# Performance work log

Measured on AMD Instinct MI355X. Metric: run time of the kernel, lower is better.

Reference implementation:

```python
import jax, jax.numpy as jnp
import numpy as np

N = 100000   # nodes
E = 1600000  # directed edges
NF = 128     # n_feat
NH = 128     # n_hid
NC = 64      # n_class


def _glorot(key, fan_in, fan_out):
    lim = (6.0 / (fan_in + fan_out)) ** 0.5
    return jax.random.uniform(key, (fan_in, fan_out), dtype=jnp.float32, minval=-lim, maxval=lim)


def setup_inputs() -> dict:
    key = jax.random.key(0)
    ks = jax.random.split(key, 10)
    x = jax.random.normal(ks[0], (N, NF), dtype=jnp.float32)
    edge_index = jax.random.randint(ks[1], (2, E), 0, N, dtype=jnp.int32)
    return {
        "x": x,
        "edge_index": edge_index,
        "W_in": _glorot(ks[2], NF, NH),
        "b_in": jnp.zeros((NH,), jnp.float32),
        "W_mid0": _glorot(ks[3], NH, NH),
        "b_mid0": jnp.zeros((NH,), jnp.float32),
        "W_mid1": _glorot(ks[4], NH, NH),
        "b_mid1": jnp.zeros((NH,), jnp.float32),
        "W_out": _glorot(ks[5], NH, NC),
        "b_out": jnp.zeros((NC,), jnp.float32),
        "W_skip_out": _glorot(ks[6], NH, NC),
    }


def _gcn_conv(x, W, b, src, dst, coef, n):
    # x' = D^-1/2 (A + I) D^-1/2 (x W) + b   (symmetric-normalized GCN conv)
    h = x @ W                               # [N, out]
    msg = h[src] * coef[:, None]            # [E+N, out] gather + scale
    return jax.ops.segment_sum(msg, dst, num_segments=n) + b


def reference(x, edge_index, W_in, b_in, W_mid0, b_mid0, W_mid1, b_mid1, W_out, b_out, W_skip_out):
    loops = jnp.arange(N, dtype=edge_index.dtype)
    src = jnp.concatenate([edge_index[0], loops])  # add self-loops
    dst = jnp.concatenate([edge_index[1], loops])
    deg = jax.ops.segment_sum(jnp.ones_like(dst, dtype=jnp.float32), dst, num_segments=N)
    dinv = jax.lax.rsqrt(deg)                      # deg >= 1 due to self-loops
    coef = dinv[src] * dinv[dst]                   # [E+N]

    # in layer: conv + res skip (NF == NH so plain add) + relu; dropout is no-op in eval
    h = _gcn_conv(x, W_in, b_in, src, dst, coef, N)
    x = jax.nn.relu(h + x)
    # mid layers
    for W, b in ((W_mid0, b_mid0), (W_mid1, b_mid1)):
        h = _gcn_conv(x, W, b, src, dst, coef, N)
        x = jax.nn.relu(h + x)
    # out layer: conv + res skip with channel projection NH -> NC
    h = _gcn_conv(x, W_out, b_out, src, dst, coef, N)
    return h + x @ W_skip_out
```

## Files before the change

### kernel.cpp

```cpp
#include <hip/hip_runtime.h>
#include <hip/hip_bf16.h>

constexpr int NN = 100000;
constexpr int NE = 1600000;
constexpr int BKN  = 256;
constexpr int NB2  = (NN + BKN - 1) / BKN;
constexpr int TILE = 4096;
constexpr int NT   = (NE + TILE - 1) / TILE;

__device__ __forceinline__ unsigned short f2bf(float f) {
    unsigned int u = __float_as_uint(f);
    unsigned int r = (u + 0x7fffu + ((u >> 16) & 1u)) >> 16;
    return (unsigned short)r;
}
__device__ __forceinline__ float bflo(unsigned int u) { return __uint_as_float(u << 16); }
__device__ __forceinline__ float bfhi(unsigned int u) { return __uint_as_float(u & 0xffff0000u); }
__device__ __forceinline__ float bf2f(unsigned short h) { return __uint_as_float(((unsigned int)h) << 16); }
__device__ __forceinline__ unsigned int pack2bf(float lo, float hi) {
    return (unsigned int)f2bf(lo) | ((unsigned int)f2bf(hi) << 16);
}

typedef __bf16 v8bf __attribute__((ext_vector_type(8)));
typedef float  v4f  __attribute__((ext_vector_type(4)));
typedef float  v2f  __attribute__((ext_vector_type(2)));

__device__ __forceinline__ v2f fp8x2_to_f32(unsigned int u) {
    return __builtin_amdgcn_cvt_pk_f32_fp8(u, false);
}

constexpr size_t OFF_BCNT  = 0;
constexpr size_t OFF_BBASE = OFF_BCNT  + 2048;
constexpr size_t OFF_BCUR  = OFF_BBASE + 2048;
constexpr size_t OFF_RP    = OFF_BCUR  + 2048;
constexpr size_t OFF_DINV  = OFF_RP    + 400384;
constexpr size_t OFF_COL   = OFF_DINV  + 400384;
constexpr size_t OFF_WT    = OFF_COL   + 6400000;
constexpr size_t OFF_H8    = OFF_WT    + 32768;
constexpr size_t OFF_H     = OFF_H8    + 12800000;
constexpr size_t OFF_X     = OFF_H     + 25600000;


__global__ __launch_bounds__(256) void bhist_kernel(const int* __restrict__ edst,
                                                    int* __restrict__ bcnt) {
    __shared__ int h[NB2];
    for (int i = threadIdx.x; i < NB2; i += 256) h[i] = 0;
    __syncthreads();
    const int base = blockIdx.x * TILE;
    #pragma unroll
    for (int j = 0; j < 16; ++j) {
        int e = base + j * 256 + threadIdx.x;
        if (e < NE) atomicAdd(&h[edst[e] >> 8], 1);
    }
    __syncthreads();
    for (int i = threadIdx.x; i < NB2; i += 256)
        if (h[i]) atomicAdd(&bcnt[i], h[i]);
}

__global__ __launch_bounds__(512) void bscan_kernel(const int* __restrict__ bcnt,
                                                    int* __restrict__ bbase,
                                                    int* __restrict__ bcur) {
    __shared__ int s[512];
    const int t = threadIdx.x;
    int v = (t < NB2) ? bcnt[t] : 0;
    s[t] = v;
    __syncthreads();
    for (int off = 1; off < 512; off <<= 1) {
        int a = (t >= off) ? s[t - off] : 0;
        __syncthreads();
        s[t] += a;
        __syncthreads();
    }
    int excl = s[t] - v;
    if (t < NB2) { bbase[t] = excl; bcur[t] = excl; }
    if (t == NB2 - 1) bbase[NB2] = excl + v;
}

__global__ __launch_bounds__(256) void scatter2_kernel(const int* __restrict__ esrc,
                                                       const int* __restrict__ edst,
                                                       int* __restrict__ bcur,
                                                       unsigned int* __restrict__ ebuf) {
    __shared__ int h[NB2];
    __shared__ int cur[NB2];
    for (int i = threadIdx.x; i < NB2; i += 256) h[i] = 0;
    __syncthreads();
    const int base = blockIdx.x * TILE;
    #pragma unroll
    for (int j = 0; j < 16; ++j) {
        int e = base + j * 256 + threadIdx.x;
        if (e < NE) atomicAdd(&h[edst[e] >> 8], 1);
    }
    __syncthreads();
    for (int i = threadIdx.x; i < NB2; i += 256) {
        int c = h[i];
        cur[i] = c ? atomicAdd(&bcur[i], c) : 0;
    }
    __syncthreads();
    #pragma unroll
    for (int j = 0; j < 16; ++j) {
        int e = base + j * 256 + threadIdx.x;
        if (e < NE) {
            int s = esrc[e], d = edst[e];
            int pos = atomicAdd(&cur[d >> 8], 1);
            ebuf[pos] = (unsigned int)s | ((unsigned int)(d & 255) << 24);
        }
    }
}

__global__ __launch_bounds__(256) void csrfill2_kernel(const unsigned int* __restrict__ ebuf,
                                                       const int* __restrict__ bbase,
                                                       int* __restrict__ rp,
                                                       float* __restrict__ dinv,
                                                       int* __restrict__ col) {
    __shared__ int cnt[256];
    __shared__ int cursor[256];
    __shared__ int s[256];
    __shared__ int sbeg, send;
    const int b = blockIdx.x;
    const int t = threadIdx.x;
    if (t == 0) { sbeg = bbase[b]; send = bbase[b + 1]; }
    cnt[t] = 0;
    __syncthreads();
    const int beg = sbeg, end = send;
    const int node0 = b * BKN;

    for (int e = beg + t; e < end; e += 256)
        atomicAdd(&cnt[ebuf[e] >> 24], 1);
    __syncthreads();

    int v = cnt[t];
    s[t] = v;
    __syncthreads();
    for (int off = 1; off < 256; off <<= 1) {
        int a = (t >= off) ? s[t - off] : 0;
        __syncthreads();
        s[t] += a;
        __syncthreads();
    }
    int excl = s[t] - v;
    int gnode = node0 + t;
    if (gnode < NN) {
        rp[gnode]   = beg + excl;
        dinv[gnode] = rsqrtf((float)(v + 1));
    }
    cursor[t] = beg + excl;
    if (b == NB2 - 1 && t == 0) rp[NN] = NE;
    __syncthreads();

    for (int e = beg + t; e < end; e += 256) {
        unsigned int sd = ebuf[e];
        int pos = atomicAdd(&cursor[sd >> 24], 1);
        col[pos] = (int)(sd & 0xFFFFFFu);
    }
}

__global__ __launch_bounds__(256) void wpre_kernel(const float* __restrict__ W0,
                                                   const float* __restrict__ W1,
                                                   int wstride,
                                                   unsigned short* __restrict__ Wt) {
    int e = blockIdx.x * 256 + threadIdx.x;
    int k = e >> 7, c = e & 127;
    float v = (c < 64) ? W0[(size_t)k * wstride + c] : W1[(size_t)k * wstride + (c - 64)];
    Wt[c * 128 + k] = f2bf(v);
}

constexpr int XROW = 136;

template<bool XF32, bool OUT8>
__global__ __launch_bounds__(256) void gemm_mfma_kernel(const void* __restrict__ Xv,
                                                        const unsigned short* __restrict__ Wt,
                                                        const float* __restrict__ dinv,
                                                        int scaleMask,
                                                        void* __restrict__ Ho) {
    __shared__ unsigned short Wl[128 * XROW];
    __shared__ unsigned short Xl[64 * XROW];

    const int t = threadIdx.x;
    const int rowBase = blockIdx.x * 64;

    #pragma unroll
    for (int i = 0; i < 8; ++i) {
        int f = i * 256 + t;
        int r = f >> 4, c8 = f & 15;
        uint4 w = *(const uint4*)&Wt[r * 128 + c8 * 8];
        *(uint4*)&Wl[r * XROW + c8 * 8] = w;
    }
    if (XF32) {
        const float* X = (const float*)Xv;
        #pragma unroll
        for (int i = 0; i < 8; ++i) {
            int f = i * 256 + t;
            int r = f >> 5, c4 = f & 31;
            int gn = rowBase + r;
            float4 v = make_float4(0.f, 0.f, 0.f, 0.f);
            if (gn < NN) v = *(const float4*)&X[(size_t)gn * 128 + c4 * 4];
            ushort4 o;
            o.x = f2bf(v.x); o.y = f2bf(v.y); o.z = f2bf(v.z); o.w = f2bf(v.w);
            *(ushort4*)&Xl[r * XROW + c4 * 4] = o;
        }
    } else {
        const unsigned short* X = (const unsigned short*)Xv;
        #pragma unroll
        for (int i = 0; i < 4; ++i) {
            int f = i * 256 + t;
            int r = f >> 4, c8 = f & 15;
            int gn = rowBase + r;
            uint4 v = make_uint4(0u, 0u, 0u, 0u);
            if (gn < NN) v = *(const uint4*)&X[(size_t)gn * 128 + c8 * 8];
            *(uint4*)&Xl[r * XROW + c8 * 8] = v;
        }
    }
    __syncthreads();

    const int w  = t >> 6;
    const int l  = t & 63;
    const int lr = l & 15;
    const int lk = (l >> 4) * 8;

    v4f acc[8];
    #pragma unroll
    for (int n = 0; n < 8; ++n) acc[n] = (v4f){0.f, 0.f, 0.f, 0.f};

    const unsigned short* ax = &Xl[(w * 16 + lr) * XROW + lk];
    const unsigned short* bx = &Wl[lr * XROW + lk];

    #pragma unroll
    for (int kk = 0; kk < 4; ++kk) {
        v8bf a = *(const v8bf*)&ax[kk * 32];
        #pragma unroll
        for (int n = 0; n < 8; ++n) {
            v8bf b = *(const v8bf*)&bx[(n * 16) * XROW + kk * 32];
            acc[n] = __builtin_amdgcn_mfma_f32_16x16x32_bf16(a, b, acc[n], 0, 0, 0);
        }
    }

    #pragma unroll
    for (int r_ = 0; r_ < 4; ++r_) {
        int row  = w * 16 + (l >> 4) * 4 + r_;
        int grow = rowBase + row;
        float dsc = dinv[grow < NN ? grow : NN - 1];
        #pragma unroll
        for (int n = 0; n < 8; ++n) {
            float sc = ((scaleMask >> (n >> 2)) & 1) ? dsc : 1.f;
            Xl[row * XROW + n * 16 + lr] = f2bf(acc[n][r_] * sc);
        }
    }
    __syncthreads();

    if (OUT8) {
        unsigned char* H8 = (unsigned char*)Ho;
        #pragma unroll
        for (int i = 0; i < 4; ++i) {
            int f = i * 256 + t;
            int r = f >> 4, c8 = f & 15;
            int gn = rowBase + r;
            if (gn < NN) {
                uint4 v = *(const uint4*)&Xl[r * XROW + c8 * 8];
                unsigned int lo = __builtin_amdgcn_cvt_pk_fp8_f32(bflo(v.x), bfhi(v.x), 0u, false);
                lo = __builtin_amdgcn_cvt_pk_fp8_f32(bflo(v.y), bfhi(v.y), lo, true);
                unsigned int hi = __builtin_amdgcn_cvt_pk_fp8_f32(bflo(v.z), bfhi(v.z), 0u, false);
                hi = __builtin_amdgcn_cvt_pk_fp8_f32(bflo(v.w), bfhi(v.w), hi, true);
                *(uint2*)&H8[(size_t)gn * 128 + c8 * 8] = make_uint2(lo, hi);
            }
        }
    } else {
        unsigned short* Hb = (unsigned short*)Ho;
        #pragma unroll
        for (int i = 0; i < 4; ++i) {
            int f = i * 256 + t;
            int r = f >> 4, c8 = f & 15;
            int gn = rowBase + r;
            if (gn < NN) {
                uint4 v = *(const uint4*)&Xl[r * XROW + c8 * 8];
                *(uint4*)&Hb[(size_t)gn * 128 + c8 * 8] = v;
            }
        }
    }
}

template<bool XF32>
__global__ __launch_bounds__(256) void agg128_kernel(const unsigned char* __restrict__ H8,
                                                     const void* __restrict__ Xoldv,
                                                     const int* __restrict__ rp,
                                                     const int* __restrict__ col,
                                                     const float* __restrict__ dinv,
                                                     const float* __restrict__ bias,
                                                     unsigned int* __restrict__ Xnew) {
    const int wid  = threadIdx.x >> 6;
    const int lane = threadIdx.x & 63;
    const int i = blockIdx.x * 4 + wid;
    if (i >= NN) return;

    const unsigned short* __restrict__ Hs = (const unsigned short*)H8;

    const float di = dinv[i];
    const float2 b2 = ((const float2*)bias)[lane];
    float xox, xoy;
    if (XF32) {
        float2 xo = ((const float2*)Xoldv)[(size_t)i * 64 + lane];
        xox = xo.x; xoy = xo.y;
    } else {
        unsigned int xo = ((const unsigned int*)Xoldv)[(size_t)i * 64 + lane];
        xox = bflo(xo); xoy = bfhi(xo);
    }

    v2f sf = fp8x2_to_f32(Hs[(size_t)i * 64 + lane]);
    float ax = sf.x, ay = sf.y;

    const int beg = rp[i], end = rp[i + 1];
    int e = beg;
    for (; e + 8 <= end; e += 8) {
        int s0 = col[e],     s1 = col[e + 1], s2 = col[e + 2], s3 = col[e + 3];
        int s4 = col[e + 4], s5 = col[e + 5], s6 = col[e + 6], s7 = col[e + 7];
        unsigned int u0 = Hs[(size_t)s0 * 64 + lane];
        unsigned int u1 = Hs[(size_t)s1 * 64 + lane];
        unsigned int u2 = Hs[(size_t)s2 * 64 + lane];
        unsigned int u3 = Hs[(size_t)s3 * 64 + lane];
        unsigned int u4 = Hs[(size_t)s4 * 64 + lane];
        unsigned int u5 = Hs[(size_t)s5 * 64 + lane];
        unsigned int u6 = Hs[(size_t)s6 * 64 + lane];
        unsigned int u7 = Hs[(size_t)s7 * 64 + lane];
        v2f m0 = fp8x2_to_f32(u0), m1 = fp8x2_to_f32(u1);
        v2f m2 = fp8x2_to_f32(u2), m3 = fp8x2_to_f32(u3);
        v2f m4 = fp8x2_to_f32(u4), m5 = fp8x2_to_f32(u5);
        v2f m6 = fp8x2_to_f32(u6), m7 = fp8x2_to_f32(u7);
        ax += ((m0.x + m1.x) + (m2.x + m3.x)) + ((m4.x + m5.x) + (m6.x + m7.x));
        ay += ((m0.y + m1.y) + (m2.y + m3.y)) + ((m4.y + m5.y) + (m6.y + m7.y));
    }
    for (; e + 4 <= end; e += 4) {
        int s0 = col[e], s1 = col[e + 1], s2 = col[e + 2], s3 = col[e + 3];
        unsigned int u0 = Hs[(size_t)s0 * 64 + lane];
        unsigned int u1 = Hs[(size_t)s1 * 64 + lane];
        unsigned int u2 = Hs[(size_t)s2 * 64 + lane];
        unsigned int u3 = Hs[(size_t)s3 * 64 + lane];
        v2f m0 = fp8x2_to_f32(u0), m1 = fp8x2_to_f32(u1);
        v2f m2 = fp8x2_to_f32(u2), m3 = fp8x2_to_f32(u3);
        ax += (m0.x + m1.x) + (m2.x + m3.x);
        ay += (m0.y + m1.y) + (m2.y + m3.y);
    }
    for (; e < end; ++e) {
        v2f m = fp8x2_to_f32(Hs[(size_t)col[e] * 64 + lane]);
        ax += m.x;
        ay += m.y;
    }

    float ox = fmaxf(di * ax + b2.x + xox, 0.f);
    float oy = fmaxf(di * ay + b2.y + xoy, 0.f);
    Xnew[(size_t)i * 64 + lane] = pack2bf(ox, oy);
}

__global__ __launch_bounds__(256) void aggout_kernel(const unsigned short* __restrict__ Hb,
                                                     const int* __restrict__ rp,
                                                     const int* __restrict__ col,
                                                     const float* __restrict__ dinv,
                                                     const float* __restrict__ bias,
                                                     float* __restrict__ out) {
    const int wid  = threadIdx.x >> 6;
    const int lane = threadIdx.x & 63;
    const int i = blockIdx.x * 4 + wid;
    if (i >= NN) return;

    const float di = dinv[i];
    const float b  = bias[lane];
    const float sk = bf2f(Hb[(size_t)i * 128 + 64 + lane]);

    float a = bf2f(Hb[(size_t)i * 128 + lane]);
    const int beg = rp[i], end = rp[i + 1];
    int e = beg;
    for (; e + 8 <= end; e += 8) {
        int s0 = col[e],     s1 = col[e + 1], s2 = col[e + 2], s3 = col[e + 3];
        int s4 = col[e + 4], s5 = col[e + 5], s6 = col[e + 6], s7 = col[e + 7];
        float m0 = bf2f(Hb[(size_t)s0 * 128 + lane]);
        float m1 = bf2f(Hb[(size_t)s1 * 128 + lane]);
        float m2 = bf2f(Hb[(size_t)s2 * 128 + lane]);
        float m3 = bf2f(Hb[(size_t)s3 * 128 + lane]);
        float m4 = bf2f(Hb[(size_t)s4 * 128 + lane]);
        float m5 = bf2f(Hb[(size_t)s5 * 128 + lane]);
        float m6 = bf2f(Hb[(size_t)s6 * 128 + lane]);
        float m7 = bf2f(Hb[(size_t)s7 * 128 + lane]);
        a += ((m0 + m1) + (m2 + m3)) + ((m4 + m5) + (m6 + m7));
    }
    for (; e + 4 <= end; e += 4) {
        int s0 = col[e], s1 = col[e + 1], s2 = col[e + 2], s3 = col[e + 3];
        float m0 = bf2f(Hb[(size_t)s0 * 128 + lane]);
        float m1 = bf2f(Hb[(size_t)s1 * 128 + lane]);
        float m2 = bf2f(Hb[(size_t)s2 * 128 + lane]);
        float m3 = bf2f(Hb[(size_t)s3 * 128 + lane]);
        a += (m0 + m1) + (m2 + m3);
    }
    for (; e < end; ++e) a += bf2f(Hb[(size_t)col[e] * 128 + lane]);

    out[(size_t)i * 64 + lane] = di * a + b + sk;
}

extern "C" void kernel_launch(void* const* d_in, const int* in_sizes, int n_in,
                              void* d_out, int out_size, void* d_ws, size_t ws_size,
                              hipStream_t stream) {
    const float* x      = (const float*)d_in[0];
    const int*   ei     = (const int*)d_in[1];
    const float* W_in   = (const float*)d_in[2];
    const float* b_in   = (const float*)d_in[3];
    const float* W_mid0 = (const float*)d_in[4];
    const float* b_mid0 = (const float*)d_in[5];
    const float* W_mid1 = (const float*)d_in[6];
    const float* b_mid1 = (const float*)d_in[7];
    const float* W_out  = (const float*)d_in[8];
    const float* b_out  = (const float*)d_in[9];
    const float* W_skip = (const float*)d_in[10];

    const int* esrc = ei;
    const int* edst = ei + NE;

    char* ws = (char*)d_ws;
    int*   bcnt   = (int*)  (ws + OFF_BCNT);
    int*   bbase  = (int*)  (ws + OFF_BBASE);
    int*   bcur   = (int*)  (ws + OFF_BCUR);
    int*   rp     = (int*)  (ws + OFF_RP);
    float* dinv   = (float*)(ws + OFF_DINV);
    int*   col    = (int*)  (ws + OFF_COL);
    unsigned short* wt   = (unsigned short*)(ws + OFF_WT);
    unsigned char*  h8   = (unsigned char*) (ws + OFF_H8);
    unsigned short* hbuf = (unsigned short*)(ws + OFF_H);
    unsigned int*   ebuf = (unsigned int*)  (ws + OFF_H);
    unsigned short* xbuf = (unsigned short*)(ws + OFF_X);
    unsigned int*   xbufw = (unsigned int*) (ws + OFF_X);
    float* outp   = (float*)d_out;

    const int gemmGrid = (NN + 63) / 64;
    const int aggGrid  = (NN + 3) / 4;

    hipMemsetAsync(bcnt, 0, (size_t)(NB2 + 1) * 4, stream);
    bhist_kernel<<<NT, 256, 0, stream>>>(edst, bcnt);
    bscan_kernel<<<1, 512, 0, stream>>>(bcnt, bbase, bcur);
    scatter2_kernel<<<NT, 256, 0, stream>>>(esrc, edst, bcur, ebuf);
    csrfill2_kernel<<<NB2, 256, 0, stream>>>(ebuf, bbase, rp, dinv, col);

    wpre_kernel<<<64, 256, 0, stream>>>(W_in, W_in + 64, 128, wt);
    gemm_mfma_kernel<true, true><<<gemmGrid, 256, 0, stream>>>(x, wt, dinv, 3, h8);
    agg128_kernel<true><<<aggGrid, 256, 0, stream>>>(h8, x, rp, col, dinv, b_in, xbufw);

    wpre_kernel<<<64, 256, 0, stream>>>(W_mid0, W_mid0 + 64, 128, wt);
    gemm_mfma_kernel<false, true><<<gemmGrid, 256, 0, stream>>>(xbuf, wt, dinv, 3, h8);
    agg128_kernel<false><<<aggGrid, 256, 0, stream>>>(h8, xbuf, rp, col, dinv, b_mid0, xbufw);

    wpre_kernel<<<64, 256, 0, stream>>>(W_mid1, W_mid1 + 64, 128, wt);
    gemm_mfma_kernel<false, true><<<gemmGrid, 256, 0, stream>>>(xbuf, wt, dinv, 3, h8);
    agg128_kernel<false><<<aggGrid, 256, 0, stream>>>(h8, xbuf, rp, col, dinv, b_mid1, xbufw);

    wpre_kernel<<<64, 256, 0, stream>>>(W_out, W_skip, 64, wt);
    gemm_mfma_kernel<false, false><<<gemmGrid, 256, 0, stream>>>(xbuf, wt, dinv, 1, hbuf);
    aggout_kernel<<<aggGrid, 256, 0, stream>>>(hbuf, rp, col, dinv, b_out, outp);
}
```

Baseline: 339.5 us.

## Store output-layer messages as FP8 with separate skip buffer, unroll aggregation to 16

The final GEMM now writes the 64 message columns as FP8 into a compact 64-byte-per-row buffer and the skip projection as bf16 in a separate buffer. The output aggregation then gathers single FP8 bytes instead of bf16 values from a 256-byte stride. This cuts gather traffic and the cache footprint of the last layer. The hidden-layer aggregation loop is also unrolled from 8 to 16 neighbours to put more loads in flight. Together these risk extra output-layer quantization error and higher register pressure.

```diff
diff --git a/kernel.cpp b/kernel.cpp
--- a/kernel.cpp
+++ b/kernel.cpp
@@ -25,7 +25,12 @@
 typedef float  v2f  __attribute__((ext_vector_type(2)));
 
 __device__ __forceinline__ v2f fp8x2_to_f32(unsigned int u) {
-    return __builtin_amdgcn_cvt_pk_f32_fp8(u, false);
+    v2f t = __builtin_amdgcn_cvt_pk_f32_fp8(u, false);
+    return t;
+}
+__device__ __forceinline__ float fp8b(unsigned char b) {
+    v2f t = __builtin_amdgcn_cvt_pk_f32_fp8((unsigned int)b, false);
+    return t.x;
 }
 
 constexpr size_t OFF_BCNT  = 0;
@@ -165,7 +170,7 @@
 
 constexpr int XROW = 136;
 
-template<bool XF32, bool OUT8>
+template<bool XF32, int OMODE>
 __global__ __launch_bounds__(256) void gemm_mfma_kernel(const void* __restrict__ Xv,
                                                         const unsigned short* __restrict__ Wt,
                                                         const float* __restrict__ dinv,
@@ -246,7 +251,7 @@
     }
     __syncthreads();
 
-    if (OUT8) {
+    if (OMODE == 1) {
         unsigned char* H8 = (unsigned char*)Ho;
         #pragma unroll
         for (int i = 0; i < 4; ++i) {
@@ -263,7 +268,8 @@
             }
         }
     } else {
-        unsigned short* Hb = (unsigned short*)Ho;
+        unsigned char*  h8o   = (unsigned char*)Ho;
+        unsigned short* skipb = (unsigned short*)((char*)Ho + (size_t)NN * 64);
         #pragma unroll
         for (int i = 0; i < 4; ++i) {
             int f = i * 256 + t;
@@ -271,7 +277,15 @@
             int gn = rowBase + r;
             if (gn < NN) {
                 uint4 v = *(const uint4*)&Xl[r * XROW + c8 * 8];
-                *(uint4*)&Hb[(size_t)gn * 128 + c8 * 8] = v;
+                if (c8 < 8) {
+                    unsigned int lo = __builtin_amdgcn_cvt_pk_fp8_f32(bflo(v.x), bfhi(v.x), 0u, false);
+                    lo = __builtin_amdgcn_cvt_pk_fp8_f32(bflo(v.y), bfhi(v.y), lo, true);
+                    unsigned int hi = __builtin_amdgcn_cvt_pk_fp8_f32(bflo(v.z), bfhi(v.z), 0u, false);
+                    hi = __builtin_amdgcn_cvt_pk_fp8_f32(bflo(v.w), bfhi(v.w), hi, true);
+                    *(uint2*)&h8o[(size_t)gn * 64 + c8 * 8] = make_uint2(lo, hi);
+                } else {
+                    *(uint4*)&skipb[(size_t)gn * 64 + (c8 - 8) * 8] = v;
+                }
             }
         }
     }
@@ -308,30 +322,23 @@
 
     const int beg = rp[i], end = rp[i + 1];
     int e = beg;
-    for (; e + 8 <= end; e += 8) {
-        int s0 = col[e],     s1 = col[e + 1], s2 = col[e + 2], s3 = col[e + 3];
-        int s4 = col[e + 4], s5 = col[e + 5], s6 = col[e + 6], s7 = col[e + 7];
-        unsigned int u0 = Hs[(size_t)s0 * 64 + lane];
-        unsigned int u1 = Hs[(size_t)s1 * 64 + lane];
-        unsigned int u2 = Hs[(size_t)s2 * 64 + lane];
-        unsigned int u3 = Hs[(size_t)s3 * 64 + lane];
-        unsigned int u4 = Hs[(size_t)s4 * 64 + lane];
-        unsigned int u5 = Hs[(size_t)s5 * 64 + lane];
-        unsigned int u6 = Hs[(size_t)s6 * 64 + lane];
-        unsigned int u7 = Hs[(size_t)s7 * 64 + lane];
-        v2f m0 = fp8x2_to_f32(u0), m1 = fp8x2_to_f32(u1);
-        v2f m2 = fp8x2_to_f32(u2), m3 = fp8x2_to_f32(u3);
-        v2f m4 = fp8x2_to_f32(u4), m5 = fp8x2_to_f32(u5);
-        v2f m6 = fp8x2_to_f32(u6), m7 = fp8x2_to_f32(u7);
-        ax += ((m0.x + m1.x) + (m2.x + m3.x)) + ((m4.x + m5.x) + (m6.x + m7.x));
-        ay += ((m0.y + m1.y) + (m2.y + m3.y)) + ((m4.y + m5.y) + (m6.y + m7.y));
+    for (; e + 16 <= end; e += 16) {
+        unsigned int u[16];
+        #pragma unroll
+        for (int j = 0; j < 16; ++j) u[j] = Hs[(size_t)col[e + j] * 64 + lane];
+        v2f m[16];
+        #pragma unroll
+        for (int j = 0; j < 16; ++j) m[j] = fp8x2_to_f32(u[j]);
+        v2f s01 = ((m[0] + m[1]) + (m[2] + m[3])) + ((m[4] + m[5]) + (m[6] + m[7]));
+        v2f s02 = ((m[8] + m[9]) + (m[10] + m[11])) + ((m[12] + m[13]) + (m[14] + m[15]));
+        ax += s01.x + s02.x;
+        ay += s01.y + s02.y;
     }
     for (; e + 4 <= end; e += 4) {
-        int s0 = col[e], s1 = col[e + 1], s2 = col[e + 2], s3 = col[e + 3];
-        unsigned int u0 = Hs[(size_t)s0 * 64 + lane];
-        unsigned int u1 = Hs[(size_t)s1 * 64 + lane];
-        unsigned int u2 = Hs[(size_t)s2 * 64 + lane];
-        unsigned int u3 = Hs[(size_t)s3 * 64 + lane];
+        unsigned int u0 = Hs[(size_t)col[e]     * 64 + lane];
+        unsigned int u1 = Hs[(size_t)col[e + 1] * 64 + lane];
+        unsigned int u2 = Hs[(size_t)col[e + 2] * 64 + lane];
+        unsigned int u3 = Hs[(size_t)col[e + 3] * 64 + lane];
         v2f m0 = fp8x2_to_f32(u0), m1 = fp8x2_to_f32(u1);
         v2f m2 = fp8x2_to_f32(u2), m3 = fp8x2_to_f32(u3);
         ax += (m0.x + m1.x) + (m2.x + m3.x);
@@ -348,7 +355,8 @@
     Xnew[(size_t)i * 64 + lane] = pack2bf(ox, oy);
 }
 
-__global__ __launch_bounds__(256) void aggout_kernel(const unsigned short* __restrict__ Hb,
+__global__ __launch_bounds__(256) void aggout_kernel(const unsigned char* __restrict__ h8o,
+                                                     const unsigned short* __restrict__ skipb,
                                                      const int* __restrict__ rp,
                                                      const int* __restrict__ col,
                                                      const float* __restrict__ dinv,
@@ -361,33 +369,31 @@
 
     const float di = dinv[i];
     const float b  = bias[lane];
-    const float sk = bf2f(Hb[(size_t)i * 128 + 64 + lane]);
-
-    float a = bf2f(Hb[(size_t)i * 128 + lane]);
+    const float sk = bf2f(skipb[(size_t)i * 64 + lane]);
+
+    float a = fp8b(h8o[(size_t)i * 64 + lane]);
     const int beg = rp[i], end = rp[i + 1];
     int e = beg;
     for (; e + 8 <= end; e += 8) {
-        int s0 = col[e],     s1 = col[e + 1], s2 = col[e + 2], s3 = col[e + 3];
-        int s4 = col[e + 4], s5 = col[e + 5], s6 = col[e + 6], s7 = col[e + 7];
-        float m0 = bf2f(Hb[(size_t)s0 * 128 + lane]);
-        float m1 = bf2f(Hb[(size_t)s1 * 128 + lane]);
-        float m2 = bf2f(Hb[(size_t)s2 * 128 + lane]);
-        float m3 = bf2f(Hb[(size_t)s3 * 128 + lane]);
-        float m4 = bf2f(Hb[(size_t)s4 * 128 + lane]);
-        float m5 = bf2f(Hb[(size_t)s5 * 128 + lane]);
-        float m6 = bf2f(Hb[(size_t)s6 * 128 + lane]);
-        float m7 = bf2f(Hb[(size_t)s7 * 128 + lane]);
-        a += ((m0 + m1) + (m2 + m3)) + ((m4 + m5) + (m6 + m7));
+        unsigned char c0 = h8o[(size_t)col[e]     * 64 + lane];
+        unsigned char c1 = h8o[(size_t)col[e + 1] * 64 + lane];
+        unsigned char c2 = h8o[(size_t)col[e + 2] * 64 + lane];
+        unsigned char c3 = h8o[(size_t)col[e + 3] * 64 + lane];
+        unsigned char c4 = h8o[(size_t)col[e + 4] * 64 + lane];
+        unsigned char c5 = h8o[(size_t)col[e + 5] * 64 + lane];
+        unsigned char c6 = h8o[(size_t)col[e + 6] * 64 + lane];
+        unsigned char c7 = h8o[(size_t)col[e + 7] * 64 + lane];
+        a += ((fp8b(c0) + fp8b(c1)) + (fp8b(c2) + fp8b(c3))) +
+             ((fp8b(c4) + fp8b(c5)) + (fp8b(c6) + fp8b(c7)));
     }
     for (; e + 4 <= end; e += 4) {
-        int s0 = col[e], s1 = col[e + 1], s2 = col[e + 2], s3 = col[e + 3];
-        float m0 = bf2f(Hb[(size_t)s0 * 128 + lane]);
-        float m1 = bf2f(Hb[(size_t)s1 * 128 + lane]);
-        float m2 = bf2f(Hb[(size_t)s2 * 128 + lane]);
-        float m3 = bf2f(Hb[(size_t)s3 * 128 + lane]);
-        a += (m0 + m1) + (m2 + m3);
-    }
-    for (; e < end; ++e) a += bf2f(Hb[(size_t)col[e] * 128 + lane]);
+        unsigned char c0 = h8o[(size_t)col[e]     * 64 + lane];
+        unsigned char c1 = h8o[(size_t)col[e + 1] * 64 + lane];
+        unsigned char c2 = h8o[(size_t)col[e + 2] * 64 + lane];
+        unsigned char c3 = h8o[(size_t)col[e + 3] * 64 + lane];
+        a += (fp8b(c0) + fp8b(c1)) + (fp8b(c2) + fp8b(c3));
+    }
+    for (; e < end; ++e) a += fp8b(h8o[(size_t)col[e] * 64 + lane]);
 
     out[(size_t)i * 64 + lane] = di * a + b + sk;
 }
@@ -419,7 +425,8 @@
     int*   col    = (int*)  (ws + OFF_COL);
     unsigned short* wt   = (unsigned short*)(ws + OFF_WT);
     unsigned char*  h8   = (unsigned char*) (ws + OFF_H8);
-    unsigned short* hbuf = (unsigned short*)(ws + OFF_H);
+    unsigned char*  h8o  = (unsigned char*) (ws + OFF_H);
+    unsigned short* skipb = (unsigned short*)(ws + OFF_H + (size_t)NN * 64);
     unsigned int*   ebuf = (unsigned int*)  (ws + OFF_H);
     unsigned short* xbuf = (unsigned short*)(ws + OFF_X);
     unsigned int*   xbufw = (unsigned int*) (ws + OFF_X);
@@ -428,25 +435,25 @@
     const int gemmGrid = (NN + 63) / 64;
     const int aggGrid  = (NN + 3) / 4;
 
-    hipMemsetAsync(bcnt, 0, (size_t)(NB2 + 1) * 4, stream);
+    (void)hipMemsetAsync(bcnt, 0, (size_t)(NB2 + 1) * 4, stream);
     bhist_kernel<<<NT, 256, 0, stream>>>(edst, bcnt);
     bscan_kernel<<<1, 512, 0, stream>>>(bcnt, bbase, bcur);
     scatter2_kernel<<<NT, 256, 0, stream>>>(esrc, edst, bcur, ebuf);
     csrfill2_kernel<<<NB2, 256, 0, stream>>>(ebuf, bbase, rp, dinv, col);
 
     wpre_kernel<<<64, 256, 0, stream>>>(W_in, W_in + 64, 128, wt);
-    gemm_mfma_kernel<true, true><<<gemmGrid, 256, 0, stream>>>(x, wt, dinv, 3, h8);
+    gemm_mfma_kernel<true, 1><<<gemmGrid, 256, 0, stream>>>(x, wt, dinv, 3, h8);
     agg128_kernel<true><<<aggGrid, 256, 0, stream>>>(h8, x, rp, col, dinv, b_in, xbufw);
 
     wpre_kernel<<<64, 256, 0, stream>>>(W_mid0, W_mid0 + 64, 128, wt);
-    gemm_mfma_kernel<false, true><<<gemmGrid, 256, 0, stream>>>(xbuf, wt, dinv, 3, h8);
+    gemm_mfma_kernel<false, 1><<<gemmGrid, 256, 0, stream>>>(xbuf, wt, dinv, 3, h8);
     agg128_kernel<false><<<aggGrid, 256, 0, stream>>>(h8, xbuf, rp, col, dinv, b_mid0, xbufw);
 
     wpre_kernel<<<64, 256, 0, stream>>>(W_mid1, W_mid1 + 64, 128, wt);
-    gemm_mfma_kernel<false, true><<<gemmGrid, 256, 0, stream>>>(xbuf, wt, dinv, 3, h8);
+    gemm_mfma_kernel<false, 1><<<gemmGrid, 256, 0, stream>>>(xbuf, wt, dinv, 3, h8);
     agg128_kernel<false><<<aggGrid, 256, 0, stream>>>(h8, xbuf, rp, col, dinv, b_mid1, xbufw);
 
     wpre_kernel<<<64, 256, 0, stream>>>(W_out, W_skip, 64, wt);
-    gemm_mfma_kernel<false, false><<<gemmGrid, 256, 0, stream>>>(xbuf, wt, dinv, 1, hbuf);
-    aggout_kernel<<<aggGrid, 256, 0, stream>>>(hbuf, rp, col, dinv, b_out, outp);
-}
+    gemm_mfma_kernel<false, 2><<<gemmGrid, 256, 0, stream>>>(xbuf, wt, dinv, 1, (void*)h8o);
+    aggout_kernel<<<aggGrid, 256, 0, stream>>>(h8o, skipb, rp, col, dinv, b_out, outp);
+}
```

Measured after the change: 340.2 us. No clear change (+0.2%).
